# Performance work log

Measured on AMD Instinct MI355X. Metric: run time of the kernel, lower is better.

The kernel has to match this reference:

```python
import jax, jax.numpy as jnp
import numpy as np


def setup_inputs() -> dict:
    key = jax.random.key(0)
    ks = jax.random.split(key, 6)
    Q, S, D, C = 128, 512, 768, 64
    return {
        "query_reps": jax.random.normal(ks[0], (Q, D), dtype=jnp.float32),
        "support_reps": jax.random.normal(ks[1], (S, D), dtype=jnp.float32),
        "W1": jax.random.normal(ks[2], (2 * D, 2 * D), dtype=jnp.float32) * 0.02,
        "b1": jnp.zeros((2 * D,), dtype=jnp.float32),
        "W2": jax.random.normal(ks[3], (1, 2 * D), dtype=jnp.float32) * 0.02,
        "b2": jnp.zeros((1,), dtype=jnp.float32),
        "support_labels": jnp.sort(jax.random.randint(ks[4], (S,), 0, C)),
        "query_target_ids": jax.random.randint(ks[5], (Q,), 0, C),
        "num_classes": C,
    }


def reference(query_reps, support_reps, W1, b1, W2, b2,
              support_labels, query_target_ids, num_classes):
    D = query_reps.shape[1]
    # Original: concat_reps = cat([repeat_interleave(q, S), s.repeat(Q)], dim=1)
    # then relu(Linear_2Dx2D(concat)). Equivalent split-weight form avoids the
    # explicit [Q*S, 2D] concat: x @ W1.T = q @ W1[:, :D].T + s @ W1[:, D:].T
    hq = query_reps @ W1[:, :D].T        # [Q, 2D]
    hs = support_reps @ W1[:, D:].T      # [S, 2D]
    h = jax.nn.relu(hq[:, None, :] + hs[None, :, :] + b1)   # [Q, S, 2D]
    scores = jnp.einsum('qsd,d->qs', h, W2[0]) + b2[0]       # [Q, S]
    # aggregate_scores_by_label with support_reduction='score':
    # M one-hot [C, S] row-normalized (p=1) => per-label mean of scores.
    seg = jax.ops.segment_sum(scores.T, support_labels,
                              num_segments=num_classes).T     # [Q, C]
    counts = jax.ops.segment_sum(jnp.ones((support_labels.shape[0],), jnp.float32),
                                 support_labels, num_segments=num_classes)
    agg = seg / jnp.maximum(counts, 1.0)                      # [Q, C]
    logp = jax.nn.log_softmax(agg, axis=1)
    loss = -jnp.mean(jnp.take_along_axis(logp, query_target_ids[:, None], axis=1))
    preds = jnp.argmax(agg, axis=1)
    return (loss, preds == query_target_ids)
```

## Files before the change

### kernel.cpp

```cpp
#include <hip/hip_runtime.h>
#include <math.h>

#define QN 128
#define SN 512
#define DN 768
#define TDN 1536
#define CN 64

#define HQP_ELEMS (2 * QN * TDN)
#define HSP_ELEMS (2 * SN * TDN)
#define SPART_ELEMS (16 * QN * SN)

__global__ __launch_bounds__(256) void gemm_split_kernel(
    const float* __restrict__ query, const float* __restrict__ support,
    const float* __restrict__ W1, float* __restrict__ hqp, float* __restrict__ hsp)
{
    const int nt = blockIdx.x;
    const int mt = blockIdx.y;
    const int kz = blockIdx.z;

    const float* A;
    float* Cout;
    int M0, Koff;
    if (mt < 2) { A = query;   M0 = mt * 64;       Koff = 0;  Cout = hqp + (size_t)kz * QN * TDN; }
    else        { A = support; M0 = (mt - 2) * 64; Koff = DN; Cout = hsp + (size_t)kz * SN * TDN; }

    const int tid  = threadIdx.x;
    const int tx   = tid & 15;
    const int ty   = tid >> 4;
    const int lrow = tid >> 2;
    const int lq   = tid & 3;

    __shared__ float As[16][68];
    __shared__ float Bs[16][68];

    float acc[4][4];
    #pragma unroll
    for (int i = 0; i < 4; ++i)
        #pragma unroll
        for (int j = 0; j < 4; ++j) acc[i][j] = 0.0f;

    const int k0base = kz * 384;
    for (int k0 = k0base; k0 < k0base + 384; k0 += 16) {
        float4 av = *(const float4*)&A [(size_t)(M0 + lrow) * DN  + k0 + lq * 4];
        float4 bv = *(const float4*)&W1[(size_t)(nt * 64 + lrow) * TDN + Koff + k0 + lq * 4];
        __syncthreads();
        As[lq*4+0][lrow] = av.x; As[lq*4+1][lrow] = av.y;
        As[lq*4+2][lrow] = av.z; As[lq*4+3][lrow] = av.w;
        Bs[lq*4+0][lrow] = bv.x; Bs[lq*4+1][lrow] = bv.y;
        Bs[lq*4+2][lrow] = bv.z; Bs[lq*4+3][lrow] = bv.w;
        __syncthreads();
        #pragma unroll
        for (int kk = 0; kk < 16; ++kk) {
            float4 a4 = *(const float4*)&As[kk][ty * 4];
            float4 b4 = *(const float4*)&Bs[kk][tx * 4];
            float a[4] = {a4.x, a4.y, a4.z, a4.w};
            float b[4] = {b4.x, b4.y, b4.z, b4.w};
            #pragma unroll
            for (int i = 0; i < 4; ++i)
                #pragma unroll
                for (int j = 0; j < 4; ++j)
                    acc[i][j] += a[i] * b[j];
        }
    }

    #pragma unroll
    for (int i = 0; i < 4; ++i) {
        float4 v = make_float4(acc[i][0], acc[i][1], acc[i][2], acc[i][3]);
        *(float4*)&Cout[(size_t)(M0 + ty * 4 + i) * TDN + nt * 64 + tx * 4] = v;
    }
}

__global__ __launch_bounds__(256) void score_kernel(
    const float* __restrict__ hqp, const float* __restrict__ hsp,
    const float* __restrict__ b1, const float* __restrict__ W2,
    float* __restrict__ spart)
{
    const int jc = blockIdx.x;
    const int qt = blockIdx.y;
    const int st = blockIdx.z;

    __shared__ float hqT[96][64];
    __shared__ float hsT[96][64];
    __shared__ float w2s[96];

    const int tid = threadIdx.x;

    #pragma unroll
    for (int l = 0; l < 6; ++l) {
        int idx  = tid + l * 256;
        int row  = idx / 24;
        int quad = idx - row * 24;
        int j    = jc * 96 + quad * 4;
        float4 h0 = *(const float4*)&hqp[(size_t)(qt * 64 + row) * TDN + j];
        float4 h1 = *(const float4*)&hqp[(size_t)QN * TDN + (size_t)(qt * 64 + row) * TDN + j];
        float4 bb = *(const float4*)&b1[j];
        hqT[quad*4+0][row] = h0.x + h1.x + bb.x;
        hqT[quad*4+1][row] = h0.y + h1.y + bb.y;
        hqT[quad*4+2][row] = h0.z + h1.z + bb.z;
        hqT[quad*4+3][row] = h0.w + h1.w + bb.w;
        float4 g0 = *(const float4*)&hsp[(size_t)(st * 64 + row) * TDN + j];
        float4 g1 = *(const float4*)&hsp[(size_t)SN * TDN + (size_t)(st * 64 + row) * TDN + j];
        hsT[quad*4+0][row] = g0.x + g1.x;
        hsT[quad*4+1][row] = g0.y + g1.y;
        hsT[quad*4+2][row] = g0.z + g1.z;
        hsT[quad*4+3][row] = g0.w + g1.w;
    }
    if (tid < 24) {
        float4 w = *(const float4*)&W2[jc * 96 + tid * 4];
        w2s[tid*4+0] = w.x; w2s[tid*4+1] = w.y;
        w2s[tid*4+2] = w.z; w2s[tid*4+3] = w.w;
    }
    __syncthreads();

    const int tx = tid & 15;
    const int ty = tid >> 4;
    float acc[4][4];
    #pragma unroll
    for (int i = 0; i < 4; ++i)
        #pragma unroll
        for (int j = 0; j < 4; ++j) acc[i][j] = 0.0f;

    #pragma unroll 4
    for (int jj = 0; jj < 96; ++jj) {
        float4 a4 = *(const float4*)&hqT[jj][ty * 4];
        float4 b4 = *(const float4*)&hsT[jj][tx * 4];
        float w = w2s[jj];
        float a[4] = {a4.x, a4.y, a4.z, a4.w};
        float b[4] = {b4.x, b4.y, b4.z, b4.w};
        #pragma unroll
        for (int i = 0; i < 4; ++i)
            #pragma unroll
            for (int j = 0; j < 4; ++j)
                acc[i][j] += w * fmaxf(a[i] + b[j], 0.0f);
    }

    float* outp = spart + (size_t)jc * QN * SN;
    #pragma unroll
    for (int i = 0; i < 4; ++i) {
        float4 v = make_float4(acc[i][0], acc[i][1], acc[i][2], acc[i][3]);
        *(float4*)&outp[(size_t)(qt * 64 + ty * 4 + i) * SN + st * 64 + tx * 4] = v;
    }
}

__global__ __launch_bounds__(256) void agg_kernel(
    const float* __restrict__ spart, const int* __restrict__ labels,
    const int* __restrict__ tgt, float* __restrict__ lossp, float* __restrict__ out)
{
    const int q = blockIdx.x;
    __shared__ float cls_sum[CN];
    __shared__ float cls_cnt[CN];
    __shared__ float aggs[CN];

    const int tid = threadIdx.x;
    if (tid < CN) { cls_sum[tid] = 0.0f; cls_cnt[tid] = 0.0f; }
    __syncthreads();

    #pragma unroll
    for (int r = 0; r < 2; ++r) {
        int s = tid + r * 256;
        float sc = 0.0f;
        #pragma unroll
        for (int jcc = 0; jcc < 16; ++jcc)
            sc += spart[(size_t)jcc * QN * SN + (size_t)q * SN + s];
        int lab = labels[s];
        atomicAdd(&cls_sum[lab], sc);
        atomicAdd(&cls_cnt[lab], 1.0f);
    }
    __syncthreads();

    if (tid < CN) aggs[tid] = cls_sum[tid] / fmaxf(cls_cnt[tid], 1.0f);
    __syncthreads();

    if (tid < CN) {
        float v = aggs[tid];
        float m = v;
        #pragma unroll
        for (int off = 1; off < 64; off <<= 1)
            m = fmaxf(m, __shfl_xor(m, off));
        float av = v; int am = tid;
        #pragma unroll
        for (int off = 1; off < 64; off <<= 1) {
            float ov = __shfl_xor(av, off);
            int   oi = __shfl_xor(am, off);
            if (ov > av || (ov == av && oi < am)) { av = ov; am = oi; }
        }
        float e = expf(v - m);
        #pragma unroll
        for (int off = 1; off < 64; off <<= 1)
            e += __shfl_xor(e, off);
        if (tid == 0) {
            int t = tgt[q];
            float logp = aggs[t] - m - logf(e);
            lossp[q] = -logp / (float)QN;
            out[1 + q] = (am == t) ? 1.0f : 0.0f;
        }
    }
}

__global__ __launch_bounds__(128) void loss_kernel(
    const float* __restrict__ lossp, float* __restrict__ out)
{
    const int tid = threadIdx.x;
    float v = lossp[tid];
    #pragma unroll
    for (int off = 1; off < 64; off <<= 1)
        v += __shfl_xor(v, off);
    __shared__ float partial[2];
    if ((tid & 63) == 0) partial[tid >> 6] = v;
    __syncthreads();
    if (tid == 0) out[0] = partial[0] + partial[1];
}

extern "C" void kernel_launch(void* const* d_in, const int* in_sizes, int n_in,
                              void* d_out, int out_size, void* d_ws, size_t ws_size,
                              hipStream_t stream) {
    const float* query   = (const float*)d_in[0];
    const float* support = (const float*)d_in[1];
    const float* W1      = (const float*)d_in[2];
    const float* b1      = (const float*)d_in[3];
    const float* W2      = (const float*)d_in[4];
    const int* labels = (const int*)d_in[6];
    const int* tgt    = (const int*)d_in[7];

    float* ws    = (float*)d_ws;
    float* hqp   = ws;
    float* hsp   = hqp + HQP_ELEMS;
    float* spart = hsp + HSP_ELEMS;
    float* lossp = spart + SPART_ELEMS;
    float* out   = (float*)d_out;

    hipLaunchKernelGGL(gemm_split_kernel, dim3(24, 10, 2), dim3(256), 0, stream,
                       query, support, W1, hqp, hsp);
    hipLaunchKernelGGL(score_kernel, dim3(16, 2, 8), dim3(256), 0, stream,
                       hqp, hsp, b1, W2, spart);
    hipLaunchKernelGGL(agg_kernel, dim3(128), dim3(256), 0, stream,
                       spart, labels, tgt, lossp, out);
    hipLaunchKernelGGL(loss_kernel, dim3(1), dim3(128), 0, stream,
                       lossp, out);
}
```

Measured before the change: 126.3 us.

## Fuse label aggregation into score kernel, double-buffer GEMM, merge tail kernels

The score kernel now reduces its 64x64 score tile in shared memory and atomically adds per-label run sums into a small [Q, C] buffer, so the 16-way partial score array and its re-read are gone. The agg and loss kernels are merged into a single one-block finale that counts labels, normalises, and computes the softmax loss and argmax. The split GEMM gains double-buffered shared tiles so the next global load overlaps compute, with one barrier per step. The cost is global float atomics (nondeterministic summation order), an extra memset, and a serial single-block finale.

Result: slower. 163.4 us (+29.3%).

```diff
diff --git a/kernel.cpp b/kernel.cpp
--- a/kernel.cpp
+++ b/kernel.cpp
@@ -9,7 +9,6 @@
 
 #define HQP_ELEMS (2 * QN * TDN)
 #define HSP_ELEMS (2 * SN * TDN)
-#define SPART_ELEMS (16 * QN * SN)
 
 __global__ __launch_bounds__(256) void gemm_split_kernel(
     const float* __restrict__ query, const float* __restrict__ support,
@@ -31,8 +30,8 @@
     const int lrow = tid >> 2;
     const int lq   = tid & 3;
 
-    __shared__ float As[16][68];
-    __shared__ float Bs[16][68];
+    __shared__ float As[2][16][68];
+    __shared__ float Bs[2][16][68];
 
     float acc[4][4];
     #pragma unroll
@@ -40,20 +39,30 @@
         #pragma unroll
         for (int j = 0; j < 4; ++j) acc[i][j] = 0.0f;
 
-    const int k0base = kz * 384;
-    for (int k0 = k0base; k0 < k0base + 384; k0 += 16) {
-        float4 av = *(const float4*)&A [(size_t)(M0 + lrow) * DN  + k0 + lq * 4];
-        float4 bv = *(const float4*)&W1[(size_t)(nt * 64 + lrow) * TDN + Koff + k0 + lq * 4];
-        __syncthreads();
-        As[lq*4+0][lrow] = av.x; As[lq*4+1][lrow] = av.y;
-        As[lq*4+2][lrow] = av.z; As[lq*4+3][lrow] = av.w;
-        Bs[lq*4+0][lrow] = bv.x; Bs[lq*4+1][lrow] = bv.y;
-        Bs[lq*4+2][lrow] = bv.z; Bs[lq*4+3][lrow] = bv.w;
-        __syncthreads();
+    const float* Aptr = &A [(size_t)(M0 + lrow) * DN  + kz * 384 + lq * 4];
+    const float* Bptr = &W1[(size_t)(nt * 64 + lrow) * TDN + Koff + kz * 384 + lq * 4];
+
+    {
+        float4 av = *(const float4*)(Aptr);
+        float4 bv = *(const float4*)(Bptr);
+        As[0][lq*4+0][lrow] = av.x; As[0][lq*4+1][lrow] = av.y;
+        As[0][lq*4+2][lrow] = av.z; As[0][lq*4+3][lrow] = av.w;
+        Bs[0][lq*4+0][lrow] = bv.x; Bs[0][lq*4+1][lrow] = bv.y;
+        Bs[0][lq*4+2][lrow] = bv.z; Bs[0][lq*4+3][lrow] = bv.w;
+    }
+    __syncthreads();
+
+    int buf = 0;
+    for (int it = 0; it < 24; ++it) {
+        float4 av, bv;
+        if (it < 23) {
+            av = *(const float4*)(Aptr + (it + 1) * 16);
+            bv = *(const float4*)(Bptr + (it + 1) * 16);
+        }
         #pragma unroll
         for (int kk = 0; kk < 16; ++kk) {
-            float4 a4 = *(const float4*)&As[kk][ty * 4];
-            float4 b4 = *(const float4*)&Bs[kk][tx * 4];
+            float4 a4 = *(const float4*)&As[buf][kk][ty * 4];
+            float4 b4 = *(const float4*)&Bs[buf][kk][tx * 4];
             float a[4] = {a4.x, a4.y, a4.z, a4.w};
             float b[4] = {b4.x, b4.y, b4.z, b4.w};
             #pragma unroll
@@ -62,6 +71,15 @@
                 for (int j = 0; j < 4; ++j)
                     acc[i][j] += a[i] * b[j];
         }
+        if (it < 23) {
+            int nb = buf ^ 1;
+            As[nb][lq*4+0][lrow] = av.x; As[nb][lq*4+1][lrow] = av.y;
+            As[nb][lq*4+2][lrow] = av.z; As[nb][lq*4+3][lrow] = av.w;
+            Bs[nb][lq*4+0][lrow] = bv.x; Bs[nb][lq*4+1][lrow] = bv.y;
+            Bs[nb][lq*4+2][lrow] = bv.z; Bs[nb][lq*4+3][lrow] = bv.w;
+            __syncthreads();
+            buf = nb;
+        }
     }
 
     #pragma unroll
@@ -74,7 +92,7 @@
 __global__ __launch_bounds__(256) void score_kernel(
     const float* __restrict__ hqp, const float* __restrict__ hsp,
     const float* __restrict__ b1, const float* __restrict__ W2,
-    float* __restrict__ spart)
+    const int* __restrict__ labels, float* __restrict__ aggbuf)
 {
     const int jc = blockIdx.x;
     const int qt = blockIdx.y;
@@ -83,8 +101,12 @@
     __shared__ float hqT[96][64];
     __shared__ float hsT[96][64];
     __shared__ float w2s[96];
+    __shared__ float sc[64][68];
+    __shared__ int   lab[64];
 
     const int tid = threadIdx.x;
+
+    if (tid < 64) lab[tid] = labels[st * 64 + tid];
 
     #pragma unroll
     for (int l = 0; l < 6; ++l) {
@@ -135,50 +157,59 @@
                 acc[i][j] += w * fmaxf(a[i] + b[j], 0.0f);
     }
 
-    float* outp = spart + (size_t)jc * QN * SN;
     #pragma unroll
     for (int i = 0; i < 4; ++i) {
         float4 v = make_float4(acc[i][0], acc[i][1], acc[i][2], acc[i][3]);
-        *(float4*)&outp[(size_t)(qt * 64 + ty * 4 + i) * SN + st * 64 + tx * 4] = v;
-    }
-}
-
-__global__ __launch_bounds__(256) void agg_kernel(
-    const float* __restrict__ spart, const int* __restrict__ labels,
-    const int* __restrict__ tgt, float* __restrict__ lossp, float* __restrict__ out)
+        *(float4*)&sc[ty * 4 + i][tx * 4] = v;
+    }
+    __syncthreads();
+
+    {
+        int row = tid >> 2;
+        int seg = tid & 3;
+        float* aggrow = aggbuf + (size_t)(qt * 64 + row) * CN;
+        int   runc = lab[seg * 16];
+        float runv = 0.0f;
+        #pragma unroll
+        for (int k = 0; k < 16; ++k) {
+            int s = seg * 16 + k;
+            int c = lab[s];
+            if (c != runc) {
+                atomicAdd(&aggrow[runc], runv);
+                runv = 0.0f; runc = c;
+            }
+            runv += sc[row][s];
+        }
+        atomicAdd(&aggrow[runc], runv);
+    }
+}
+
+__global__ __launch_bounds__(256) void finale_kernel(
+    const float* __restrict__ aggbuf, const int* __restrict__ labels,
+    const int* __restrict__ tgt, float* __restrict__ out)
 {
-    const int q = blockIdx.x;
-    __shared__ float cls_sum[CN];
-    __shared__ float cls_cnt[CN];
-    __shared__ float aggs[CN];
+    __shared__ float cnt[CN];
+    __shared__ float lsum[4];
 
     const int tid = threadIdx.x;
-    if (tid < CN) { cls_sum[tid] = 0.0f; cls_cnt[tid] = 0.0f; }
-    __syncthreads();
-
-    #pragma unroll
-    for (int r = 0; r < 2; ++r) {
-        int s = tid + r * 256;
-        float sc = 0.0f;
-        #pragma unroll
-        for (int jcc = 0; jcc < 16; ++jcc)
-            sc += spart[(size_t)jcc * QN * SN + (size_t)q * SN + s];
-        int lab = labels[s];
-        atomicAdd(&cls_sum[lab], sc);
-        atomicAdd(&cls_cnt[lab], 1.0f);
-    }
-    __syncthreads();
-
-    if (tid < CN) aggs[tid] = cls_sum[tid] / fmaxf(cls_cnt[tid], 1.0f);
-    __syncthreads();
-
-    if (tid < CN) {
-        float v = aggs[tid];
+    if (tid < CN) cnt[tid] = 0.0f;
+    __syncthreads();
+    atomicAdd(&cnt[labels[tid]],       1.0f);
+    atomicAdd(&cnt[labels[tid + 256]], 1.0f);
+    __syncthreads();
+
+    const int g    = tid >> 6;
+    const int lane = tid & 63;
+    float myloss = 0.0f;
+
+    for (int it = 0; it < 32; ++it) {
+        int q = it * 4 + g;
+        float v = aggbuf[(size_t)q * CN + lane] / fmaxf(cnt[lane], 1.0f);
         float m = v;
         #pragma unroll
         for (int off = 1; off < 64; off <<= 1)
             m = fmaxf(m, __shfl_xor(m, off));
-        float av = v; int am = tid;
+        float av = v; int am = lane;
         #pragma unroll
         for (int off = 1; off < 64; off <<= 1) {
             float ov = __shfl_xor(av, off);
@@ -189,27 +220,17 @@
         #pragma unroll
         for (int off = 1; off < 64; off <<= 1)
             e += __shfl_xor(e, off);
-        if (tid == 0) {
-            int t = tgt[q];
-            float logp = aggs[t] - m - logf(e);
-            lossp[q] = -logp / (float)QN;
+        int t = tgt[q];
+        float vt = __shfl(v, t, 64);
+        if (lane == 0) {
+            myloss += -(vt - m - logf(e));
             out[1 + q] = (am == t) ? 1.0f : 0.0f;
         }
     }
-}
-
-__global__ __launch_bounds__(128) void loss_kernel(
-    const float* __restrict__ lossp, float* __restrict__ out)
-{
-    const int tid = threadIdx.x;
-    float v = lossp[tid];
-    #pragma unroll
-    for (int off = 1; off < 64; off <<= 1)
-        v += __shfl_xor(v, off);
-    __shared__ float partial[2];
-    if ((tid & 63) == 0) partial[tid >> 6] = v;
-    __syncthreads();
-    if (tid == 0) out[0] = partial[0] + partial[1];
+    if (lane == 0) lsum[g] = myloss;
+    __syncthreads();
+    if (tid == 0)
+        out[0] = (lsum[0] + lsum[1] + lsum[2] + lsum[3]) / (float)QN;
 }
 
 extern "C" void kernel_launch(void* const* d_in, const int* in_sizes, int n_in,
@@ -223,19 +244,17 @@
     const int* labels = (const int*)d_in[6];
     const int* tgt    = (const int*)d_in[7];
 
-    float* ws    = (float*)d_ws;
-    float* hqp   = ws;
-    float* hsp   = hqp + HQP_ELEMS;
-    float* spart = hsp + HSP_ELEMS;
-    float* lossp = spart + SPART_ELEMS;
-    float* out   = (float*)d_out;
-
+    float* ws     = (float*)d_ws;
+    float* hqp    = ws;
+    float* hsp    = hqp + HQP_ELEMS;
+    float* aggbuf = hsp + HSP_ELEMS;
+    float* out    = (float*)d_out;
+
+    hipMemsetAsync(aggbuf, 0, (size_t)QN * CN * sizeof(float), stream);
     hipLaunchKernelGGL(gemm_split_kernel, dim3(24, 10, 2), dim3(256), 0, stream,
                        query, support, W1, hqp, hsp);
     hipLaunchKernelGGL(score_kernel, dim3(16, 2, 8), dim3(256), 0, stream,
-                       hqp, hsp, b1, W2, spart);
-    hipLaunchKernelGGL(agg_kernel, dim3(128), dim3(256), 0, stream,
-                       spart, labels, tgt, lossp, out);
-    hipLaunchKernelGGL(loss_kernel, dim3(1), dim3(128), 0, stream,
-                       lossp, out);
-}
+                       hqp, hsp, b1, W2, labels, aggbuf);
+    hipLaunchKernelGGL(finale_kernel, dim3(1), dim3(256), 0, stream,
+                       aggbuf, labels, tgt, out);
+}
```
